# Optimization experiments

Measured on AMD Instinct MI355X. Metric: run time of the kernel, lower is better.

The kernel has to match this reference:

```python
import jax, jax.numpy as jnp
import numpy as np

B, N, V, H, R, A, IN, K = 64, 512, 64, 512, 4, 18, 128, 32
EPS = 1e-8


def setup_inputs() -> dict:
    key = jax.random.key(0)
    ks = jax.random.split(key, 20)
    g = lambda i, shape, s=1.0: jax.random.normal(ks[i], shape, jnp.float32) * s
    u = lambda i, shape: jax.random.uniform(ks[i], shape, dtype=jnp.float32)
    cin = IN + R * V
    return dict(
        x=g(0, (B, IN)),
        h=g(1, (B, H), 0.1),
        c=g(2, (B, H), 0.1),
        memory=g(3, (B, N, V), 0.1),
        read_weights=u(4, (B, R, N)),
        write_weights=u(5, (B, N)),
        usage=u(6, (B, N)),
        link_matrix=u(7, (B, N, N)) * 0.01,
        precedence_weights=u(8, (B, N)),
        W_ih=g(9, (4 * H, cin), 0.05), W_hh=g(10, (4 * H, H), 0.05),
        b_ih=jnp.zeros(4 * H, jnp.float32), b_hh=jnp.zeros(4 * H, jnp.float32),
        W_read=g(11, (R, V + 4, H), 0.05), b_read=jnp.zeros((R, V + 4), jnp.float32),
        W_write=g(12, (3 * V + 3, H), 0.05), b_write=jnp.zeros(3 * V + 3, jnp.float32),
        W_pol=g(13, (A, H), 0.05), b_pol=jnp.zeros(A, jnp.float32),
        W_val=g(14, (1, H), 0.05), b_val=jnp.zeros(1, jnp.float32),
    )


def reference(x, h, c, memory, read_weights, write_weights, usage, link_matrix,
              precedence_weights, W_ih, W_hh, b_ih, b_hh, W_read, b_read,
              W_write, b_write, W_pol, b_pol, W_val, b_val):
    # ---- read heads (vectorized over R) ----
    ro = jnp.einsum('roh,bh->bro', W_read, h) + b_read            # [B,R,V+4]
    rkey = ro[..., :V]
    rbeta = jax.nn.softplus(ro[..., V])                           # [B,R]
    rpi = jax.nn.softmax(ro[..., V + 1:V + 4], axis=-1)           # backward/content/forward gates
    mem_norm = jnp.maximum(jnp.linalg.norm(memory, axis=-1), EPS)  # [B,N]
    key_norm = jnp.maximum(jnp.linalg.norm(rkey, axis=-1), EPS)    # [B,R]
    sim = jnp.einsum('bnv,brv->brn', memory, rkey) / (mem_norm[:, None, :] * key_norm[..., None])
    scores = rbeta[..., None] * sim                                # [B,R,N]
    kth = jax.lax.top_k(scores, K)[0][..., -1:]                    # sparse top-k mask
    cw = jax.nn.softmax(jnp.where(scores >= kth, scores, -jnp.inf), axis=-1)
    fw = jnp.einsum('bnm,brm->brn', link_matrix, read_weights)     # forward weighting L w
    bw = jnp.einsum('bmn,brm->brn', link_matrix, read_weights)     # backward weighting L^T w
    w_r = rpi[..., 0:1] * bw + rpi[..., 1:2] * cw + rpi[..., 2:3] * fw  # [B,R,N]
    rvec = jnp.einsum('brn,bnv->brv', w_r, memory).reshape(B, R * V)
    # ---- LSTM controller (torch LSTMCell gate order i,f,g,o) ----
    gates = jnp.concatenate([x, rvec], -1) @ W_ih.T + h @ W_hh.T + b_ih + b_hh
    i_g, f_g, g_g, o_g = jnp.split(gates, 4, axis=-1)
    c_new = jax.nn.sigmoid(f_g) * c + jax.nn.sigmoid(i_g) * jnp.tanh(g_g)
    h_new = jax.nn.sigmoid(o_g) * jnp.tanh(c_new)
    # ---- write head ----
    wo = h_new @ W_write.T + b_write                               # [B,3V+3]
    wkey = wo[:, :V]
    erase = jax.nn.sigmoid(wo[:, V:2 * V])
    add = jnp.tanh(wo[:, 2 * V:3 * V])
    wbeta = jax.nn.softplus(wo[:, 3 * V])
    g_a = jax.nn.sigmoid(wo[:, 3 * V + 1])
    g_w = jax.nn.sigmoid(wo[:, 3 * V + 2])
    wkey_norm = jnp.maximum(jnp.linalg.norm(wkey, axis=-1), EPS)
    wsim = jnp.einsum('bnv,bv->bn', memory, wkey) / (mem_norm * wkey_norm[:, None])
    cw_w = jax.nn.softmax(wbeta[:, None] * wsim, axis=-1)
    # allocation weighting from sorted usage (DNC Eq. 1)
    idx = jnp.argsort(usage, axis=-1)
    u_sorted = jnp.take_along_axis(usage, idx, -1)
    prod_prev = jnp.concatenate([jnp.ones((B, 1), usage.dtype), jnp.cumprod(u_sorted, -1)[:, :-1]], -1)
    a_sorted = (1.0 - u_sorted) * prod_prev
    alloc = jnp.take_along_axis(a_sorted, jnp.argsort(idx, -1), -1)
    write_w = g_w[:, None] * (g_a[:, None] * alloc + (1.0 - g_a)[:, None] * cw_w)  # [B,N]
    # ---- memory erase/add ----
    mem_new = memory * (1.0 - write_w[:, :, None] * erase[:, None, :]) + write_w[:, :, None] * add[:, None, :]
    # ---- usage (psi detached as in torch.no_grad) ----
    psi = jax.lax.stop_gradient(jnp.prod(1.0 - w_r, axis=1))
    usage_new = (usage + write_weights - usage * write_weights) * psi
    # ---- link matrix + precedence ----
    ws = jnp.sum(write_w, -1, keepdims=True)
    prec_new = (1.0 - ws) * precedence_weights + write_w
    decay = (1.0 - write_w[:, :, None]) * (1.0 - write_w[:, None, :])
    link_new = decay * link_matrix + write_w[:, :, None] * precedence_weights[:, None, :]
    link_new = link_new * (1.0 - jnp.eye(N, dtype=link_new.dtype))
    # ---- actor/critic heads ----
    logits = h_new @ W_pol.T + b_pol
    value = h_new @ W_val.T + b_val
    return (logits, value, h_new, c_new, mem_new, w_r, write_w, usage_new, link_new, prec_new)
```

## Files before the change

kernel.cpp:

```cpp
#include <hip/hip_runtime.h>
#include <math.h>

constexpr int Bb = 64, Nn = 512, Vv = 64, Hh = 512, Rr = 4, Aa = 18, INp = 128, KTOP = 32;
constexpr int CIN = 384;
constexpr int WOUT = 195;
#define EPSf 1e-8f

__device__ __forceinline__ float sigmoidf(float x){ return 1.f/(1.f+expf(-x)); }
__device__ __forceinline__ float softplusf(float x){ return (x>20.f)? x : log1pf(expf(x)); }
__device__ __forceinline__ float wave_reduce(float v){
  #pragma unroll
  for(int o=32;o>0;o>>=1) v += __shfl_down(v, o, 64);
  return v;
}

__global__ void k_read_proj(const float* __restrict__ Wr, const float* __restrict__ br,
                            const float* __restrict__ h, float* __restrict__ ro) {
  int bid = blockIdx.x;
  int b = bid / 68;
  int p = (bid % 68) * 4 + (threadIdx.x >> 6);
  int lane = threadIdx.x & 63;
  const float* wrow = Wr + p * Hh;
  const float* hb = h + b * Hh;
  float acc = 0.f;
  #pragma unroll
  for (int t = 0; t < 8; ++t) { int k = lane + 64*t; acc += wrow[k] * hb[k]; }
  acc = wave_reduce(acc);
  if (lane == 0) ro[b*272 + p] = acc + br[p];
}

__global__ void k_scores(const float* __restrict__ mem, const float* __restrict__ ro,
                         float* __restrict__ scores) {
  int row = blockIdx.x*4 + (threadIdx.x>>6);
  int lane = threadIdx.x & 63;
  int b = row >> 9, n = row & 511;
  float m = mem[row*Vv + lane];
  float mn = wave_reduce(m*m);
  #pragma unroll
  for (int r = 0; r < Rr; ++r) {
    const float* rob = ro + b*272 + r*68;
    float kv = rob[lane];
    float s  = wave_reduce(m*kv);
    float k2 = wave_reduce(kv*kv);
    if (lane == 0) {
      float rbeta = softplusf(rob[64]);
      float mnc = fmaxf(sqrtf(mn), EPSf);
      float knc = fmaxf(sqrtf(k2), EPSf);
      scores[(b*Rr + r)*Nn + n] = rbeta * s / (mnc * knc);
    }
  }
}

__global__ void k_topk_cw(const float* __restrict__ scores, float* __restrict__ cw) {
  __shared__ float sv[512];
  __shared__ float so[512];
  __shared__ float red[256];
  int br = blockIdx.x;
  int tid = threadIdx.x;
  const float* srow = scores + br*Nn;
  for (int i = tid; i < 512; i += 256) { float v = srow[i]; sv[i]=v; so[i]=v; }
  __syncthreads();
  for (int k = 2; k <= 512; k <<= 1) {
    for (int j = k>>1; j > 0; j >>= 1) {
      for (int i = tid; i < 512; i += 256) {
        int ixj = i ^ j;
        if (ixj > i) {
          float a = sv[i], c = sv[ixj];
          bool descSeg = ((i & k) == 0);
          bool sw = descSeg ? (a < c) : (a > c);
          if (sw) { sv[i]=c; sv[ixj]=a; }
        }
      }
      __syncthreads();
    }
  }
  float kth = sv[KTOP-1];
  float mx = sv[0];
  float lsum = 0.f;
  for (int i = tid; i < 512; i += 256) {
    float v = so[i];
    lsum += (v >= kth) ? expf(v - mx) : 0.f;
  }
  red[tid] = lsum; __syncthreads();
  for (int s2 = 128; s2 > 0; s2 >>= 1) {
    if (tid < s2) red[tid] += red[tid+s2];
    __syncthreads();
  }
  float inv = 1.f / red[0];
  for (int i = tid; i < 512; i += 256) {
    float v = so[i];
    cw[br*Nn + i] = (v >= kth) ? expf(v - mx)*inv : 0.f;
  }
}

__global__ void k_fwbw(const float* __restrict__ link, const float* __restrict__ rw,
                       float* __restrict__ fw, float* __restrict__ bwpart) {
  __shared__ float bl[4][4][512];
  int b  = blockIdx.x >> 3;
  int ch = blockIdx.x & 7;
  int wv = threadIdx.x >> 6, lane = threadIdx.x & 63;
  const float* rwb = rw + b*Rr*Nn;
  float rwv[4][8];
  #pragma unroll
  for (int r = 0; r < 4; ++r)
    #pragma unroll
    for (int t = 0; t < 8; ++t) rwv[r][t] = rwb[r*512 + lane + 64*t];
  float bwacc[8][4] = {};
  const float* lb = link + (size_t)b*Nn*Nn;
  int n0 = ch*64 + wv*16;
  for (int i = 0; i < 16; ++i) {
    int n = n0 + i;
    float lk[8];
    #pragma unroll
    for (int t = 0; t < 8; ++t) lk[t] = lb[n*512 + lane + 64*t];
    float s0 = rwb[n], s1 = rwb[512+n], s2 = rwb[1024+n], s3 = rwb[1536+n];
    float f0=0,f1=0,f2=0,f3=0;
    #pragma unroll
    for (int t = 0; t < 8; ++t) {
      float lv = lk[t];
      f0 += lv*rwv[0][t]; f1 += lv*rwv[1][t]; f2 += lv*rwv[2][t]; f3 += lv*rwv[3][t];
      bwacc[t][0] += lv*s0; bwacc[t][1] += lv*s1; bwacc[t][2] += lv*s2; bwacc[t][3] += lv*s3;
    }
    f0 = wave_reduce(f0); f1 = wave_reduce(f1);
    f2 = wave_reduce(f2); f3 = wave_reduce(f3);
    if (lane == 0) {
      fw[(b*Rr+0)*Nn+n] = f0; fw[(b*Rr+1)*Nn+n] = f1;
      fw[(b*Rr+2)*Nn+n] = f2; fw[(b*Rr+3)*Nn+n] = f3;
    }
  }
  #pragma unroll
  for (int t = 0; t < 8; ++t)
    #pragma unroll
    for (int r = 0; r < 4; ++r) bl[wv][r][lane + 64*t] = bwacc[t][r];
  __syncthreads();
  int tid = threadIdx.x;
  #pragma unroll
  for (int q = 0; q < 8; ++q) {
    int idx = q*256 + tid;
    int r = idx >> 9, j = idx & 511;
    float v = bl[0][r][j] + bl[1][r][j] + bl[2][r][j] + bl[3][r][j];
    bwpart[((size_t)(ch*Bb + b)*Rr + r)*Nn + j] = v;
  }
}

__global__ void k_wr_usage(const float* __restrict__ bwpart, const float* __restrict__ cw,
                           const float* __restrict__ fw, const float* __restrict__ ro,
                           const float* __restrict__ usage, const float* __restrict__ wwt,
                           float* __restrict__ out_wr, float* __restrict__ out_usage,
                           float* __restrict__ ws_rvec) {
  int idx = blockIdx.x*256 + threadIdx.x;
  if (idx < Bb*Rr*Vv) ws_rvec[idx] = 0.f;
  int b = idx >> 9, n = idx & 511;
  float psi = 1.f;
  #pragma unroll
  for (int r = 0; r < Rr; ++r) {
    int br = b*Rr + r;
    const float* rob = ro + b*272 + r*68;
    float e0 = rob[65], e1 = rob[66], e2 = rob[67];
    float m = fmaxf(e0, fmaxf(e1, e2));
    float x0 = expf(e0-m), x1 = expf(e1-m), x2 = expf(e2-m);
    float inv = 1.f/(x0+x1+x2);
    float bwv = 0.f;
    #pragma unroll
    for (int chh = 0; chh < 8; ++chh)
      bwv += bwpart[((size_t)(chh*Bb + b)*Rr + r)*Nn + n];
    float w = (x0*bwv + x1*cw[br*Nn+n] + x2*fw[br*Nn+n]) * inv;
    out_wr[br*Nn+n] = w;
    psi *= (1.f - w);
  }
  float u = usage[idx], wt = wwt[idx];
  out_usage[idx] = (u + wt - u*wt) * psi;
}

__global__ void k_rvec(const float* __restrict__ wr, const float* __restrict__ mem,
                       float* __restrict__ rvec) {
  int b = blockIdx.x >> 3;
  int ch = blockIdx.x & 7;
  int r = threadIdx.x >> 6, v = threadIdx.x & 63;
  const float* wrow = wr + (b*Rr + r)*Nn;
  const float* mb = mem + (size_t)b*Nn*Vv;
  float acc = 0.f;
  #pragma unroll 4
  for (int t = 0; t < 64; ++t) {
    int n = ch*64 + t;
    acc += wrow[n] * mb[n*Vv + v];
  }
  atomicAdd(&rvec[(b*Rr+r)*Vv + v], acc);
}

__global__ void k_gates(const float* __restrict__ x, const float* __restrict__ rvec,
                        const float* __restrict__ h, const float* __restrict__ Wih,
                        const float* __restrict__ Whh, const float* __restrict__ bih,
                        const float* __restrict__ bhh, float* __restrict__ gates) {
  int gid = blockIdx.x*4 + (threadIdx.x>>6);
  int lane = threadIdx.x & 63;
  int jt = gid >> 4;
  int bt = gid & 15;
  float acc[4][4] = {};
  #pragma unroll
  for (int t = 0; t < 6; ++t) {
    int k = lane + 64*t;
    float u[4], w[4];
    #pragma unroll
    for (int i = 0; i < 4; ++i) {
      int b = bt*4 + i;
      u[i] = (k < INp) ? x[b*INp + k] : rvec[b*(Rr*Vv) + k - INp];
      w[i] = Wih[(jt*4+i)*CIN + k];
    }
    #pragma unroll
    for (int jj = 0; jj < 4; ++jj)
      #pragma unroll
      for (int bb = 0; bb < 4; ++bb) acc[jj][bb] += w[jj]*u[bb];
  }
  #pragma unroll
  for (int t = 0; t < 8; ++t) {
    int k = lane + 64*t;
    float u[4], w[4];
    #pragma unroll
    for (int i = 0; i < 4; ++i) {
      u[i] = h[(bt*4+i)*Hh + k];
      w[i] = Whh[(jt*4+i)*Hh + k];
    }
    #pragma unroll
    for (int jj = 0; jj < 4; ++jj)
      #pragma unroll
      for (int bb = 0; bb < 4; ++bb) acc[jj][bb] += w[jj]*u[bb];
  }
  #pragma unroll
  for (int jj = 0; jj < 4; ++jj)
    #pragma unroll
    for (int bb = 0; bb < 4; ++bb) {
      float v = wave_reduce(acc[jj][bb]);
      if (lane == 0) {
        int j = jt*4 + jj, b = bt*4 + bb;
        gates[b*(4*Hh) + j] = v + bih[j] + bhh[j];
      }
    }
}

__global__ void k_lstm(const float* __restrict__ gates, const float* __restrict__ c,
                       float* __restrict__ out_h, float* __restrict__ out_c) {
  int idx = blockIdx.x*256 + threadIdx.x;
  int b = idx >> 9, hh = idx & 511;
  const float* g = gates + b*2048;
  float ig = sigmoidf(g[hh]), fg = sigmoidf(g[512+hh]);
  float gg = tanhf(g[1024+hh]), og = sigmoidf(g[1536+hh]);
  float cn = fg * c[idx] + ig * gg;
  float hn = og * tanhf(cn);
  out_c[idx] = cn; out_h[idx] = hn;
}

__global__ void k_wopol(const float* __restrict__ hn, const float* __restrict__ Ww,
                        const float* __restrict__ bw_, const float* __restrict__ Wp,
                        const float* __restrict__ bp, const float* __restrict__ Wv,
                        const float* __restrict__ bv, float* __restrict__ wo,
                        float* __restrict__ out_logits, float* __restrict__ out_value) {
  int gid = blockIdx.x*4 + (threadIdx.x>>6);
  int lane = threadIdx.x & 63;
  int b = gid / 214, o = gid % 214;
  const float* wrow;
  if (o < WOUT) wrow = Ww + o*Hh;
  else if (o < WOUT + Aa) wrow = Wp + (o-WOUT)*Hh;
  else wrow = Wv;
  const float* hb = hn + b*Hh;
  float acc = 0.f;
  #pragma unroll
  for (int t = 0; t < 8; ++t) { int k = lane+64*t; acc += hb[k]*wrow[k]; }
  acc = wave_reduce(acc);
  if (lane == 0) {
    if (o < WOUT) wo[b*WOUT+o] = acc + bw_[o];
    else if (o < WOUT + Aa) out_logits[b*Aa + (o-WOUT)] = acc + bp[o-WOUT];
    else out_value[b] = acc + bv[0];
  }
}

__global__ void k_wsim(const float* __restrict__ mem, const float* __restrict__ wo,
                       float* __restrict__ wsim) {
  int row = blockIdx.x*4 + (threadIdx.x>>6);
  int lane = threadIdx.x & 63;
  int b = row >> 9;
  const float* wob = wo + b*WOUT;
  float kv = wob[lane];
  float m = mem[row*Vv + lane];
  float s  = wave_reduce(m*kv);
  float mn = wave_reduce(m*m);
  float k2 = wave_reduce(kv*kv);
  if (lane == 0) {
    float wbeta = softplusf(wob[192]);
    wsim[row] = wbeta * s / (fmaxf(sqrtf(mn),EPSf) * fmaxf(sqrtf(k2),EPSf));
  }
}

__global__ void k_alloc(const float* __restrict__ usage, const float* __restrict__ wo,
                        const float* __restrict__ wsim, const float* __restrict__ prec,
                        float* __restrict__ out_ww, float* __restrict__ out_prec) {
  __shared__ float uv[512];
  __shared__ int   ui[512];
  __shared__ float cp[512];
  __shared__ float al[512];
  __shared__ float red[256];
  int b = blockIdx.x, tid = threadIdx.x;
  float s0 = wsim[b*Nn + tid], s1 = wsim[b*Nn + tid + 256];
  red[tid] = fmaxf(s0, s1); __syncthreads();
  for (int s2=128; s2>0; s2>>=1){ if (tid<s2) red[tid]=fmaxf(red[tid],red[tid+s2]); __syncthreads(); }
  float mx = red[0]; __syncthreads();
  float e0 = expf(s0-mx), e1 = expf(s1-mx);
  red[tid] = e0+e1; __syncthreads();
  for (int s2=128; s2>0; s2>>=1){ if (tid<s2) red[tid]+=red[tid+s2]; __syncthreads(); }
  float cinv = 1.f/red[0];
  float c0 = e0*cinv, c1 = e1*cinv;
  __syncthreads();
  for (int i = tid; i < 512; i += 256) { uv[i] = usage[b*Nn+i]; ui[i] = i; }
  __syncthreads();
  for (int k = 2; k <= 512; k <<= 1) {
    for (int j = k>>1; j > 0; j >>= 1) {
      for (int i = tid; i < 512; i += 256) {
        int ixj = i ^ j;
        if (ixj > i) {
          float av = uv[i], bv = uv[ixj];
          int ai = ui[i], bi = ui[ixj];
          bool gt = (av > bv) || (av == bv && ai > bi);
          bool asc = ((i & k) == 0);
          bool sw = asc ? gt : !gt;
          if (sw) { uv[i]=bv; uv[ixj]=av; ui[i]=bi; ui[ixj]=ai; }
        }
      }
      __syncthreads();
    }
  }
  for (int i = tid; i < 512; i += 256) cp[i] = uv[i];
  __syncthreads();
  for (int d = 1; d < 512; d <<= 1) {
    float t0 = cp[tid]     * ((tid >= d)     ? cp[tid-d]     : 1.f);
    float t1 = cp[tid+256] * ((tid+256 >= d) ? cp[tid+256-d] : 1.f);
    __syncthreads();
    cp[tid] = t0; cp[tid+256] = t1;
    __syncthreads();
  }
  for (int i = tid; i < 512; i += 256) {
    float pp = (i == 0) ? 1.f : cp[i-1];
    al[ui[i]] = (1.f - uv[i]) * pp;
  }
  __syncthreads();
  float ga = sigmoidf(wo[b*WOUT+193]);
  float gw = sigmoidf(wo[b*WOUT+194]);
  int n0 = tid, n1 = tid+256;
  float wv0 = gw * (ga*al[n0] + (1.f-ga)*c0);
  float wv1 = gw * (ga*al[n1] + (1.f-ga)*c1);
  out_ww[b*Nn+n0] = wv0; out_ww[b*Nn+n1] = wv1;
  red[tid] = wv0 + wv1; __syncthreads();
  for (int s2=128; s2>0; s2>>=1){ if (tid<s2) red[tid]+=red[tid+s2]; __syncthreads(); }
  float wsum = red[0];
  out_prec[b*Nn+n0] = (1.f - wsum)*prec[b*Nn+n0] + wv0;
  out_prec[b*Nn+n1] = (1.f - wsum)*prec[b*Nn+n1] + wv1;
}

__global__ void k_memlink(const float* __restrict__ link, const float* __restrict__ ww,
                          const float* __restrict__ prec, const float* __restrict__ mem,
                          const float* __restrict__ wo, float* __restrict__ out_link,
                          float* __restrict__ out_mem) {
  int bid = blockIdx.x;
  if (bid < 16384) {
    int idx4 = bid*256 + threadIdx.x;
    int base = idx4*4;
    int b = base >> 18;
    int rem = base & 262143;
    int i = rem >> 9;
    int j0 = rem & 511;
    float wi = ww[b*Nn + i];
    float fi = 1.f - wi;
    float4 lv = *(const float4*)(link + base);
    float4 wj = *(const float4*)(ww + b*Nn + j0);
    float4 pj = *(const float4*)(prec + b*Nn + j0);
    float4 o;
    o.x = fi*(1.f-wj.x)*lv.x + wi*pj.x;
    o.y = fi*(1.f-wj.y)*lv.y + wi*pj.y;
    o.z = fi*(1.f-wj.z)*lv.z + wi*pj.z;
    o.w = fi*(1.f-wj.w)*lv.w + wi*pj.w;
    if (i >= j0 && i < j0+4) {
      if (i == j0) o.x = 0.f;
      else if (i == j0+1) o.y = 0.f;
      else if (i == j0+2) o.z = 0.f;
      else o.w = 0.f;
    }
    *(float4*)(out_link + base) = o;
  } else {
    int idx4 = (bid - 16384)*256 + threadIdx.x;
    int base = idx4*4;
    int b = base >> 15;
    int rem = base & 32767;
    int n = rem >> 6;
    int v0 = rem & 63;
    float w = ww[b*Nn + n];
    const float* wob = wo + b*WOUT;
    float4 m = *(const float4*)(mem + base);
    float4 o;
    float e, a;
    e = sigmoidf(wob[64+v0+0]); a = tanhf(wob[128+v0+0]); o.x = m.x*(1.f-w*e)+w*a;
    e = sigmoidf(wob[64+v0+1]); a = tanhf(wob[128+v0+1]); o.y = m.y*(1.f-w*e)+w*a;
    e = sigmoidf(wob[64+v0+2]); a = tanhf(wob[128+v0+2]); o.z = m.z*(1.f-w*e)+w*a;
    e = sigmoidf(wob[64+v0+3]); a = tanhf(wob[128+v0+3]); o.w = m.w*(1.f-w*e)+w*a;
    *(float4*)(out_mem + base) = o;
  }
}

extern "C" void kernel_launch(void* const* d_in, const int* in_sizes, int n_in,
                              void* d_out, int out_size, void* d_ws, size_t ws_size,
                              hipStream_t stream) {
  const float* x    = (const float*)d_in[0];
  const float* h    = (const float*)d_in[1];
  const float* c    = (const float*)d_in[2];
  const float* mem  = (const float*)d_in[3];
  const float* rw   = (const float*)d_in[4];
  const float* wwt  = (const float*)d_in[5];
  const float* usage= (const float*)d_in[6];
  const float* link = (const float*)d_in[7];
  const float* prec = (const float*)d_in[8];
  const float* Wih  = (const float*)d_in[9];
  const float* Whh  = (const float*)d_in[10];
  const float* bih  = (const float*)d_in[11];
  const float* bhh  = (const float*)d_in[12];
  const float* Wr   = (const float*)d_in[13];
  const float* br   = (const float*)d_in[14];
  const float* Ww   = (const float*)d_in[15];
  const float* bw_  = (const float*)d_in[16];
  const float* Wp   = (const float*)d_in[17];
  const float* bp   = (const float*)d_in[18];
  const float* Wv   = (const float*)d_in[19];
  const float* bv   = (const float*)d_in[20];

  float* out = (float*)d_out;
  float* o_logits = out + 0;
  float* o_value  = out + 1152;
  float* o_h      = out + 1216;
  float* o_c      = out + 33984;
  float* o_mem    = out + 66752;
  float* o_wr     = out + 2163904;
  float* o_ww     = out + 2294976;
  float* o_usage  = out + 2327744;
  float* o_link   = out + 2360512;
  float* o_prec   = out + 19137728;

  float* ws = (float*)d_ws;
  float* ws_ro     = ws;
  float* ws_sc     = ws + 17408;
  float* ws_cw     = ws + 148480;
  float* ws_fw     = ws + 279552;
  float* ws_bwpart = ws + 410624;
  float* ws_rvec   = ws + 1459200;
  float* ws_gates  = ws + 1475584;
  float* ws_wo     = ws + 1606656;
  float* ws_wsim   = ws + 1619136;

  k_read_proj <<<dim3(Bb*68),        dim3(256), 0, stream>>>(Wr, br, h, ws_ro);
  k_scores    <<<dim3(Bb*Nn/4),      dim3(256), 0, stream>>>(mem, ws_ro, ws_sc);
  k_topk_cw   <<<dim3(Bb*Rr),        dim3(256), 0, stream>>>(ws_sc, ws_cw);
  k_fwbw      <<<dim3(Bb*8),         dim3(256), 0, stream>>>(link, rw, ws_fw, ws_bwpart);
  k_wr_usage  <<<dim3(Bb*Nn/256),    dim3(256), 0, stream>>>(ws_bwpart, ws_cw, ws_fw, ws_ro, usage, wwt, o_wr, o_usage, ws_rvec);
  k_rvec      <<<dim3(Bb*8),         dim3(256), 0, stream>>>(o_wr, mem, ws_rvec);
  k_gates     <<<dim3(2048),         dim3(256), 0, stream>>>(x, ws_rvec, h, Wih, Whh, bih, bhh, ws_gates);
  k_lstm      <<<dim3(Bb*Hh/256),    dim3(256), 0, stream>>>(ws_gates, c, o_h, o_c);
  k_wopol     <<<dim3(Bb*214/4),     dim3(256), 0, stream>>>(o_h, Ww, bw_, Wp, bp, Wv, bv, ws_wo, o_logits, o_value);
  k_wsim      <<<dim3(Bb*Nn/4),      dim3(256), 0, stream>>>(mem, ws_wo, ws_wsim);
  k_alloc     <<<dim3(Bb),           dim3(256), 0, stream>>>(usage, ws_wo, ws_wsim, prec, o_ww, o_prec);
  k_memlink   <<<dim3(16384+2048),   dim3(256), 0, stream>>>(link, o_ww, prec, mem, ws_wo, o_link, o_mem);
}
```

Measured before the change: 345.2 us.

## Fuse all DNC stages into one cooperative persistent kernel with grid syncs

```diff
diff --git a/kernel.cpp b/kernel.cpp
--- a/kernel.cpp
+++ b/kernel.cpp
@@ -1,9 +1,15 @@
 #include <hip/hip_runtime.h>
+#include <hip/hip_cooperative_groups.h>
 #include <math.h>
+
+namespace cg = cooperative_groups;
 
 constexpr int Bb = 64, Nn = 512, Vv = 64, Hh = 512, Rr = 4, Aa = 18, INp = 128, KTOP = 32;
 constexpr int CIN = 384;
 constexpr int WOUT = 195;
+constexpr int GRID = 256;
+constexpr int NWAVE = GRID*4;
+constexpr int NTHRD = GRID*256;
 #define EPSf 1e-8f
 
 __device__ __forceinline__ float sigmoidf(float x){ return 1.f/(1.f+expf(-x)); }
@@ -14,393 +20,422 @@
   return v;
 }
 
-__global__ void k_read_proj(const float* __restrict__ Wr, const float* __restrict__ br,
-                            const float* __restrict__ h, float* __restrict__ ro) {
-  int bid = blockIdx.x;
-  int b = bid / 68;
-  int p = (bid % 68) * 4 + (threadIdx.x >> 6);
-  int lane = threadIdx.x & 63;
-  const float* wrow = Wr + p * Hh;
-  const float* hb = h + b * Hh;
-  float acc = 0.f;
-  #pragma unroll
-  for (int t = 0; t < 8; ++t) { int k = lane + 64*t; acc += wrow[k] * hb[k]; }
-  acc = wave_reduce(acc);
-  if (lane == 0) ro[b*272 + p] = acc + br[p];
-}
-
-__global__ void k_scores(const float* __restrict__ mem, const float* __restrict__ ro,
-                         float* __restrict__ scores) {
-  int row = blockIdx.x*4 + (threadIdx.x>>6);
-  int lane = threadIdx.x & 63;
-  int b = row >> 9, n = row & 511;
-  float m = mem[row*Vv + lane];
-  float mn = wave_reduce(m*m);
-  #pragma unroll
-  for (int r = 0; r < Rr; ++r) {
-    const float* rob = ro + b*272 + r*68;
-    float kv = rob[lane];
+constexpr int WS_RO     = 0;
+constexpr int WS_SC     = 17408;
+constexpr int WS_CW     = 148480;
+constexpr int WS_FW     = 279552;
+constexpr int WS_BWPART = 410624;
+constexpr int WS_RVEC   = 1459200;
+constexpr int WS_GATES  = 1475584;
+constexpr int WS_WO     = 1606656;
+constexpr int WS_WSIM   = 1619136;
+
+__global__ __launch_bounds__(256, 2) void dnc_mega(
+    const float* __restrict__ x, const float* __restrict__ h, const float* __restrict__ c,
+    const float* __restrict__ mem, const float* __restrict__ rw, const float* __restrict__ wwt,
+    const float* __restrict__ usage, const float* __restrict__ link, const float* __restrict__ prec,
+    const float* __restrict__ Wih, const float* __restrict__ Whh,
+    const float* __restrict__ bih, const float* __restrict__ bhh,
+    const float* __restrict__ Wr, const float* __restrict__ br,
+    const float* __restrict__ Ww, const float* __restrict__ bw_,
+    const float* __restrict__ Wp, const float* __restrict__ bp,
+    const float* __restrict__ Wv, const float* __restrict__ bv,
+    float* __restrict__ out, float* __restrict__ ws) {
+  cg::grid_group grid = cg::this_grid();
+  __shared__ __align__(16) char smem[32768];
+
+  const int tid = threadIdx.x;
+  const int wv = tid >> 6, lane = tid & 63;
+  const int blk = blockIdx.x;
+  const int gwave = blk*4 + wv;
+  const int gthread = blk*256 + tid;
+
+  float* o_logits = out + 0;
+  float* o_value  = out + 1152;
+  float* o_h      = out + 1216;
+  float* o_c      = out + 33984;
+  float* o_mem    = out + 66752;
+  float* o_wr     = out + 2163904;
+  float* o_ww     = out + 2294976;
+  float* o_usage  = out + 2327744;
+  float* o_link   = out + 2360512;
+  float* o_prec   = out + 19137728;
+
+  float* ws_ro     = ws + WS_RO;
+  float* ws_sc     = ws + WS_SC;
+  float* ws_cw     = ws + WS_CW;
+  float* ws_fw     = ws + WS_FW;
+  float* ws_bwpart = ws + WS_BWPART;
+  float* ws_rvec   = ws + WS_RVEC;
+  float* ws_gates  = ws + WS_GATES;
+  float* ws_wo     = ws + WS_WO;
+  float* ws_wsim   = ws + WS_WSIM;
+
+  for (int u = gwave; u < Bb*272; u += NWAVE) {
+    int b = u / 272, p = u % 272;
+    const float* wrow = Wr + p*Hh;
+    const float* hb = h + b*Hh;
+    float acc = 0.f;
+    #pragma unroll
+    for (int t = 0; t < 8; ++t) { int k = lane + 64*t; acc += wrow[k]*hb[k]; }
+    acc = wave_reduce(acc);
+    if (lane == 0) ws_ro[b*272 + p] = acc + br[p];
+  }
+  for (int unit = blk; unit < 512; unit += GRID) {
+    float (*bl)[4][512] = (float(*)[4][512])smem;
+    int b  = unit >> 3;
+    int ch = unit & 7;
+    const float* rwb = rw + b*Rr*Nn;
+    float rwv[4][8];
+    #pragma unroll
+    for (int r = 0; r < 4; ++r)
+      #pragma unroll
+      for (int t = 0; t < 8; ++t) rwv[r][t] = rwb[r*512 + lane + 64*t];
+    float bwacc[8][4] = {};
+    const float* lb = link + (size_t)b*Nn*Nn;
+    int n0 = ch*64 + wv*16;
+    for (int i = 0; i < 16; ++i) {
+      int n = n0 + i;
+      float lk[8];
+      #pragma unroll
+      for (int t = 0; t < 8; ++t) lk[t] = lb[n*512 + lane + 64*t];
+      float s0 = rwb[n], s1 = rwb[512+n], s2 = rwb[1024+n], s3 = rwb[1536+n];
+      float f0=0,f1=0,f2=0,f3=0;
+      #pragma unroll
+      for (int t = 0; t < 8; ++t) {
+        float lv = lk[t];
+        f0 += lv*rwv[0][t]; f1 += lv*rwv[1][t]; f2 += lv*rwv[2][t]; f3 += lv*rwv[3][t];
+        bwacc[t][0] += lv*s0; bwacc[t][1] += lv*s1; bwacc[t][2] += lv*s2; bwacc[t][3] += lv*s3;
+      }
+      f0 = wave_reduce(f0); f1 = wave_reduce(f1);
+      f2 = wave_reduce(f2); f3 = wave_reduce(f3);
+      if (lane == 0) {
+        ws_fw[(b*Rr+0)*Nn+n] = f0; ws_fw[(b*Rr+1)*Nn+n] = f1;
+        ws_fw[(b*Rr+2)*Nn+n] = f2; ws_fw[(b*Rr+3)*Nn+n] = f3;
+      }
+    }
+    #pragma unroll
+    for (int t = 0; t < 8; ++t)
+      #pragma unroll
+      for (int r = 0; r < 4; ++r) bl[wv][r][lane + 64*t] = bwacc[t][r];
+    __syncthreads();
+    #pragma unroll
+    for (int q = 0; q < 8; ++q) {
+      int idx = q*256 + tid;
+      int r = idx >> 9, j = idx & 511;
+      float v = bl[0][r][j] + bl[1][r][j] + bl[2][r][j] + bl[3][r][j];
+      ws_bwpart[((size_t)(ch*Bb + b)*Rr + r)*Nn + j] = v;
+    }
+    __syncthreads();
+  }
+  grid.sync();
+
+  for (int u = gwave; u < Bb*Nn; u += NWAVE) {
+    int b = u >> 9, n = u & 511;
+    float m = mem[u*Vv + lane];
+    float mn = wave_reduce(m*m);
+    #pragma unroll
+    for (int r = 0; r < Rr; ++r) {
+      float kv = ws_ro[b*272 + r*68 + lane];
+      float s = wave_reduce(m*kv);
+      if (lane == 0)
+        ws_sc[(b*Rr + r)*Nn + n] = s / fmaxf(sqrtf(mn), EPSf);
+    }
+  }
+  grid.sync();
+
+  {
+    float* sv = (float*)smem;
+    float* so = sv + 512;
+    float* red = so + 512;
+    float* sscale = red + 256;
+    int b = blk >> 2, r = blk & 3;
+    if (wv == 0) {
+      float kv = ws_ro[b*272 + r*68 + lane];
+      float k2 = wave_reduce(kv*kv);
+      if (lane == 0) {
+        float rbeta = softplusf(ws_ro[b*272 + r*68 + 64]);
+        *sscale = rbeta / fmaxf(sqrtf(k2), EPSf);
+      }
+    }
+    __syncthreads();
+    float scale = *sscale;
+    const float* srow = ws_sc + (b*Rr + r)*Nn;
+    for (int i = tid; i < 512; i += 256) { float v = scale*srow[i]; sv[i]=v; so[i]=v; }
+    __syncthreads();
+    for (int k = 2; k <= 512; k <<= 1) {
+      for (int j = k>>1; j > 0; j >>= 1) {
+        for (int i = tid; i < 512; i += 256) {
+          int ixj = i ^ j;
+          if (ixj > i) {
+            float a = sv[i], cc = sv[ixj];
+            bool descSeg = ((i & k) == 0);
+            bool sw = descSeg ? (a < cc) : (a > cc);
+            if (sw) { sv[i]=cc; sv[ixj]=a; }
+          }
+        }
+        __syncthreads();
+      }
+    }
+    float kth = sv[KTOP-1];
+    float mx = sv[0];
+    float lsum = 0.f;
+    for (int i = tid; i < 512; i += 256) {
+      float v = so[i];
+      lsum += (v >= kth) ? expf(v - mx) : 0.f;
+    }
+    red[tid] = lsum; __syncthreads();
+    for (int s2 = 128; s2 > 0; s2 >>= 1) {
+      if (tid < s2) red[tid] += red[tid+s2];
+      __syncthreads();
+    }
+    float inv = 1.f / red[0];
+    for (int i = tid; i < 512; i += 256) {
+      float v = so[i];
+      ws_cw[(b*Rr + r)*Nn + i] = (v >= kth) ? expf(v - mx)*inv : 0.f;
+    }
+    __syncthreads();
+  }
+  grid.sync();
+
+  if (gthread < Bb*Rr*Vv) ws_rvec[gthread] = 0.f;
+  if (gthread < Bb*Nn) {
+    int idx = gthread;
+    int b = idx >> 9, n = idx & 511;
+    float psi = 1.f;
+    #pragma unroll
+    for (int r = 0; r < Rr; ++r) {
+      int brr = b*Rr + r;
+      const float* rob = ws_ro + b*272 + r*68;
+      float e0 = rob[65], e1 = rob[66], e2 = rob[67];
+      float m = fmaxf(e0, fmaxf(e1, e2));
+      float x0 = expf(e0-m), x1 = expf(e1-m), x2 = expf(e2-m);
+      float inv = 1.f/(x0+x1+x2);
+      float bwv = 0.f;
+      #pragma unroll
+      for (int chh = 0; chh < 8; ++chh)
+        bwv += ws_bwpart[((size_t)(chh*Bb + b)*Rr + r)*Nn + n];
+      float w = (x0*bwv + x1*ws_cw[brr*Nn+n] + x2*ws_fw[brr*Nn+n]) * inv;
+      o_wr[brr*Nn+n] = w;
+      psi *= (1.f - w);
+    }
+    float u = usage[idx], wt = wwt[idx];
+    o_usage[idx] = (u + wt - u*wt) * psi;
+  }
+  grid.sync();
+
+  for (int unit = blk; unit < 512; unit += GRID) {
+    int b = unit >> 3;
+    int ch = unit & 7;
+    int r = wv, v = lane;
+    const float* wrow = o_wr + (b*Rr + r)*Nn;
+    const float* mb = mem + (size_t)b*Nn*Vv;
+    float acc = 0.f;
+    #pragma unroll 4
+    for (int t = 0; t < 64; ++t) {
+      int n = ch*64 + t;
+      acc += wrow[n] * mb[n*Vv + v];
+    }
+    atomicAdd(&ws_rvec[(b*Rr+r)*Vv + v], acc);
+  }
+  grid.sync();
+
+  for (int u = gwave; u < 8192; u += NWAVE) {
+    int jt = u >> 4;
+    int bt = u & 15;
+    float acc[4][4] = {};
+    #pragma unroll
+    for (int t = 0; t < 6; ++t) {
+      int k = lane + 64*t;
+      float uu[4], w[4];
+      #pragma unroll
+      for (int i = 0; i < 4; ++i) {
+        int b = bt*4 + i;
+        uu[i] = (k < INp) ? x[b*INp + k] : ws_rvec[b*(Rr*Vv) + k - INp];
+        w[i] = Wih[(jt*4+i)*CIN + k];
+      }
+      #pragma unroll
+      for (int jj = 0; jj < 4; ++jj)
+        #pragma unroll
+        for (int bb2 = 0; bb2 < 4; ++bb2) acc[jj][bb2] += w[jj]*uu[bb2];
+    }
+    #pragma unroll
+    for (int t = 0; t < 8; ++t) {
+      int k = lane + 64*t;
+      float uu[4], w[4];
+      #pragma unroll
+      for (int i = 0; i < 4; ++i) {
+        uu[i] = h[(bt*4+i)*Hh + k];
+        w[i] = Whh[(jt*4+i)*Hh + k];
+      }
+      #pragma unroll
+      for (int jj = 0; jj < 4; ++jj)
+        #pragma unroll
+        for (int bb2 = 0; bb2 < 4; ++bb2) acc[jj][bb2] += w[jj]*uu[bb2];
+    }
+    #pragma unroll
+    for (int jj = 0; jj < 4; ++jj)
+      #pragma unroll
+      for (int bb2 = 0; bb2 < 4; ++bb2) {
+        float v = wave_reduce(acc[jj][bb2]);
+        if (lane == 0) {
+          int j = jt*4 + jj, b = bt*4 + bb2;
+          ws_gates[b*(4*Hh) + j] = v + bih[j] + bhh[j];
+        }
+      }
+  }
+  grid.sync();
+
+  if (gthread < Bb*Hh) {
+    int idx = gthread;
+    int b = idx >> 9, hh = idx & 511;
+    const float* g = ws_gates + b*2048;
+    float ig = sigmoidf(g[hh]), fg = sigmoidf(g[512+hh]);
+    float gg = tanhf(g[1024+hh]), og = sigmoidf(g[1536+hh]);
+    float cn = fg * c[idx] + ig * gg;
+    float hn = og * tanhf(cn);
+    o_c[idx] = cn; o_h[idx] = hn;
+  }
+  grid.sync();
+
+  for (int u = gwave; u < Bb*214; u += NWAVE) {
+    int b = u / 214, o = u % 214;
+    const float* wrow;
+    if (o < WOUT) wrow = Ww + o*Hh;
+    else if (o < WOUT + Aa) wrow = Wp + (o-WOUT)*Hh;
+    else wrow = Wv;
+    const float* hb = o_h + b*Hh;
+    float acc = 0.f;
+    #pragma unroll
+    for (int t = 0; t < 8; ++t) { int k = lane+64*t; acc += hb[k]*wrow[k]; }
+    acc = wave_reduce(acc);
+    if (lane == 0) {
+      if (o < WOUT) ws_wo[b*WOUT+o] = acc + bw_[o];
+      else if (o < WOUT + Aa) o_logits[b*Aa + (o-WOUT)] = acc + bp[o-WOUT];
+      else o_value[b] = acc + bv[0];
+    }
+  }
+  grid.sync();
+
+  for (int u = gwave; u < Bb*Nn; u += NWAVE) {
+    int b = u >> 9;
+    const float* wob = ws_wo + b*WOUT;
+    float kv = wob[lane];
+    float m = mem[u*Vv + lane];
     float s  = wave_reduce(m*kv);
+    float mn = wave_reduce(m*m);
     float k2 = wave_reduce(kv*kv);
     if (lane == 0) {
-      float rbeta = softplusf(rob[64]);
-      float mnc = fmaxf(sqrtf(mn), EPSf);
-      float knc = fmaxf(sqrtf(k2), EPSf);
-      scores[(b*Rr + r)*Nn + n] = rbeta * s / (mnc * knc);
-    }
-  }
-}
-
-__global__ void k_topk_cw(const float* __restrict__ scores, float* __restrict__ cw) {
-  __shared__ float sv[512];
-  __shared__ float so[512];
-  __shared__ float red[256];
-  int br = blockIdx.x;
-  int tid = threadIdx.x;
-  const float* srow = scores + br*Nn;
-  for (int i = tid; i < 512; i += 256) { float v = srow[i]; sv[i]=v; so[i]=v; }
-  __syncthreads();
-  for (int k = 2; k <= 512; k <<= 1) {
-    for (int j = k>>1; j > 0; j >>= 1) {
-      for (int i = tid; i < 512; i += 256) {
-        int ixj = i ^ j;
-        if (ixj > i) {
-          float a = sv[i], c = sv[ixj];
-          bool descSeg = ((i & k) == 0);
-          bool sw = descSeg ? (a < c) : (a > c);
-          if (sw) { sv[i]=c; sv[ixj]=a; }
+      float wbeta = softplusf(wob[192]);
+      ws_wsim[u] = wbeta * s / (fmaxf(sqrtf(mn),EPSf) * fmaxf(sqrtf(k2),EPSf));
+    }
+  }
+  grid.sync();
+
+  if (blk < 64) {
+    float* uv = (float*)smem;
+    int*   ui = (int*)(uv + 512);
+    float* cp = (float*)(ui + 512);
+    float* al = cp + 512;
+    float* red = al + 512;
+    int b = blk;
+    float s0 = ws_wsim[b*Nn + tid], s1 = ws_wsim[b*Nn + tid + 256];
+    red[tid] = fmaxf(s0, s1); __syncthreads();
+    for (int s2=128; s2>0; s2>>=1){ if (tid<s2) red[tid]=fmaxf(red[tid],red[tid+s2]); __syncthreads(); }
+    float mx = red[0]; __syncthreads();
+    float e0 = expf(s0-mx), e1 = expf(s1-mx);
+    red[tid] = e0+e1; __syncthreads();
+    for (int s2=128; s2>0; s2>>=1){ if (tid<s2) red[tid]+=red[tid+s2]; __syncthreads(); }
+    float cinv = 1.f/red[0];
+    float c0 = e0*cinv, c1 = e1*cinv;
+    __syncthreads();
+    for (int i = tid; i < 512; i += 256) { uv[i] = usage[b*Nn+i]; ui[i] = i; }
+    __syncthreads();
+    for (int k = 2; k <= 512; k <<= 1) {
+      for (int j = k>>1; j > 0; j >>= 1) {
+        for (int i = tid; i < 512; i += 256) {
+          int ixj = i ^ j;
+          if (ixj > i) {
+            float av = uv[i], bv2 = uv[ixj];
+            int ai = ui[i], bi = ui[ixj];
+            bool gt = (av > bv2) || (av == bv2 && ai > bi);
+            bool asc = ((i & k) == 0);
+            bool sw = asc ? gt : !gt;
+            if (sw) { uv[i]=bv2; uv[ixj]=av; ui[i]=bi; ui[ixj]=ai; }
+          }
         }
-      }
+        __syncthreads();
+      }
+    }
+    for (int i = tid; i < 512; i += 256) cp[i] = uv[i];
+    __syncthreads();
+    for (int d = 1; d < 512; d <<= 1) {
+      float t0 = cp[tid]     * ((tid >= d)     ? cp[tid-d]     : 1.f);
+      float t1 = cp[tid+256] * ((tid+256 >= d) ? cp[tid+256-d] : 1.f);
       __syncthreads();
-    }
-  }
-  float kth = sv[KTOP-1];
-  float mx = sv[0];
-  float lsum = 0.f;
-  for (int i = tid; i < 512; i += 256) {
-    float v = so[i];
-    lsum += (v >= kth) ? expf(v - mx) : 0.f;
-  }
-  red[tid] = lsum; __syncthreads();
-  for (int s2 = 128; s2 > 0; s2 >>= 1) {
-    if (tid < s2) red[tid] += red[tid+s2];
-    __syncthreads();
-  }
-  float inv = 1.f / red[0];
-  for (int i = tid; i < 512; i += 256) {
-    float v = so[i];
-    cw[br*Nn + i] = (v >= kth) ? expf(v - mx)*inv : 0.f;
-  }
-}
-
-__global__ void k_fwbw(const float* __restrict__ link, const float* __restrict__ rw,
-                       float* __restrict__ fw, float* __restrict__ bwpart) {
-  __shared__ float bl[4][4][512];
-  int b  = blockIdx.x >> 3;
-  int ch = blockIdx.x & 7;
-  int wv = threadIdx.x >> 6, lane = threadIdx.x & 63;
-  const float* rwb = rw + b*Rr*Nn;
-  float rwv[4][8];
-  #pragma unroll
-  for (int r = 0; r < 4; ++r)
-    #pragma unroll
-    for (int t = 0; t < 8; ++t) rwv[r][t] = rwb[r*512 + lane + 64*t];
-  float bwacc[8][4] = {};
-  const float* lb = link + (size_t)b*Nn*Nn;
-  int n0 = ch*64 + wv*16;
-  for (int i = 0; i < 16; ++i) {
-    int n = n0 + i;
-    float lk[8];
-    #pragma unroll
-    for (int t = 0; t < 8; ++t) lk[t] = lb[n*512 + lane + 64*t];
-    float s0 = rwb[n], s1 = rwb[512+n], s2 = rwb[1024+n], s3 = rwb[1536+n];
-    float f0=0,f1=0,f2=0,f3=0;
-    #pragma unroll
-    for (int t = 0; t < 8; ++t) {
-      float lv = lk[t];
-      f0 += lv*rwv[0][t]; f1 += lv*rwv[1][t]; f2 += lv*rwv[2][t]; f3 += lv*rwv[3][t];
-      bwacc[t][0] += lv*s0; bwacc[t][1] += lv*s1; bwacc[t][2] += lv*s2; bwacc[t][3] += lv*s3;
-    }
-    f0 = wave_reduce(f0); f1 = wave_reduce(f1);
-    f2 = wave_reduce(f2); f3 = wave_reduce(f3);
-    if (lane == 0) {
-      fw[(b*Rr+0)*Nn+n] = f0; fw[(b*Rr+1)*Nn+n] = f1;
-      fw[(b*Rr+2)*Nn+n] = f2; fw[(b*Rr+3)*Nn+n] = f3;
-    }
-  }
-  #pragma unroll
-  for (int t = 0; t < 8; ++t)
-    #pragma unroll
-    for (int r = 0; r < 4; ++r) bl[wv][r][lane + 64*t] = bwacc[t][r];
-  __syncthreads();
-  int tid = threadIdx.x;
-  #pragma unroll
-  for (int q = 0; q < 8; ++q) {
-    int idx = q*256 + tid;
-    int r = idx >> 9, j = idx & 511;
-    float v = bl[0][r][j] + bl[1][r][j] + bl[2][r][j] + bl[3][r][j];
-    bwpart[((size_t)(ch*Bb + b)*Rr + r)*Nn + j] = v;
-  }
-}
-
-__global__ void k_wr_usage(const float* __restrict__ bwpart, const float* __restrict__ cw,
-                           const float* __restrict__ fw, const float* __restrict__ ro,
-                           const float* __restrict__ usage, const float* __restrict__ wwt,
-                           float* __restrict__ out_wr, float* __restrict__ out_usage,
-                           float* __restrict__ ws_rvec) {
-  int idx = blockIdx.x*256 + threadIdx.x;
-  if (idx < Bb*Rr*Vv) ws_rvec[idx] = 0.f;
-  int b = idx >> 9, n = idx & 511;
-  float psi = 1.f;
-  #pragma unroll
-  for (int r = 0; r < Rr; ++r) {
-    int br = b*Rr + r;
-    const float* rob = ro + b*272 + r*68;
-    float e0 = rob[65], e1 = rob[66], e2 = rob[67];
-    float m = fmaxf(e0, fmaxf(e1, e2));
-    float x0 = expf(e0-m), x1 = expf(e1-m), x2 = expf(e2-m);
-    float inv = 1.f/(x0+x1+x2);
-    float bwv = 0.f;
-    #pragma unroll
-    for (int chh = 0; chh < 8; ++chh)
-      bwv += bwpart[((size_t)(chh*Bb + b)*Rr + r)*Nn + n];
-    float w = (x0*bwv + x1*cw[br*Nn+n] + x2*fw[br*Nn+n]) * inv;
-    out_wr[br*Nn+n] = w;
-    psi *= (1.f - w);
-  }
-  float u = usage[idx], wt = wwt[idx];
-  out_usage[idx] = (u + wt - u*wt) * psi;
-}
-
-__global__ void k_rvec(const float* __restrict__ wr, const float* __restrict__ mem,
-                       float* __restrict__ rvec) {
-  int b = blockIdx.x >> 3;
-  int ch = blockIdx.x & 7;
-  int r = threadIdx.x >> 6, v = threadIdx.x & 63;
-  const float* wrow = wr + (b*Rr + r)*Nn;
-  const float* mb = mem + (size_t)b*Nn*Vv;
-  float acc = 0.f;
-  #pragma unroll 4
-  for (int t = 0; t < 64; ++t) {
-    int n = ch*64 + t;
-    acc += wrow[n] * mb[n*Vv + v];
-  }
-  atomicAdd(&rvec[(b*Rr+r)*Vv + v], acc);
-}
-
-__global__ void k_gates(const float* __restrict__ x, const float* __restrict__ rvec,
-                        const float* __restrict__ h, const float* __restrict__ Wih,
-                        const float* __restrict__ Whh, const float* __restrict__ bih,
-                        const float* __restrict__ bhh, float* __restrict__ gates) {
-  int gid = blockIdx.x*4 + (threadIdx.x>>6);
-  int lane = threadIdx.x & 63;
-  int jt = gid >> 4;
-  int bt = gid & 15;
-  float acc[4][4] = {};
-  #pragma unroll
-  for (int t = 0; t < 6; ++t) {
-    int k = lane + 64*t;
-    float u[4], w[4];
-    #pragma unroll
-    for (int i = 0; i < 4; ++i) {
-      int b = bt*4 + i;
-      u[i] = (k < INp) ? x[b*INp + k] : rvec[b*(Rr*Vv) + k - INp];
-      w[i] = Wih[(jt*4+i)*CIN + k];
-    }
-    #pragma unroll
-    for (int jj = 0; jj < 4; ++jj)
-      #pragma unroll
-      for (int bb = 0; bb < 4; ++bb) acc[jj][bb] += w[jj]*u[bb];
-  }
-  #pragma unroll
-  for (int t = 0; t < 8; ++t) {
-    int k = lane + 64*t;
-    float u[4], w[4];
-    #pragma unroll
-    for (int i = 0; i < 4; ++i) {
-      u[i] = h[(bt*4+i)*Hh + k];
-      w[i] = Whh[(jt*4+i)*Hh + k];
-    }
-    #pragma unroll
-    for (int jj = 0; jj < 4; ++jj)
-      #pragma unroll
-      for (int bb = 0; bb < 4; ++bb) acc[jj][bb] += w[jj]*u[bb];
-  }
-  #pragma unroll
-  for (int jj = 0; jj < 4; ++jj)
-    #pragma unroll
-    for (int bb = 0; bb < 4; ++bb) {
-      float v = wave_reduce(acc[jj][bb]);
-      if (lane == 0) {
-        int j = jt*4 + jj, b = bt*4 + bb;
-        gates[b*(4*Hh) + j] = v + bih[j] + bhh[j];
-      }
-    }
-}
-
-__global__ void k_lstm(const float* __restrict__ gates, const float* __restrict__ c,
-                       float* __restrict__ out_h, float* __restrict__ out_c) {
-  int idx = blockIdx.x*256 + threadIdx.x;
-  int b = idx >> 9, hh = idx & 511;
-  const float* g = gates + b*2048;
-  float ig = sigmoidf(g[hh]), fg = sigmoidf(g[512+hh]);
-  float gg = tanhf(g[1024+hh]), og = sigmoidf(g[1536+hh]);
-  float cn = fg * c[idx] + ig * gg;
-  float hn = og * tanhf(cn);
-  out_c[idx] = cn; out_h[idx] = hn;
-}
-
-__global__ void k_wopol(const float* __restrict__ hn, const float* __restrict__ Ww,
-                        const float* __restrict__ bw_, const float* __restrict__ Wp,
-                        const float* __restrict__ bp, const float* __restrict__ Wv,
-                        const float* __restrict__ bv, float* __restrict__ wo,
-                        float* __restrict__ out_logits, float* __restrict__ out_value) {
-  int gid = blockIdx.x*4 + (threadIdx.x>>6);
-  int lane = threadIdx.x & 63;
-  int b = gid / 214, o = gid % 214;
-  const float* wrow;
-  if (o < WOUT) wrow = Ww + o*Hh;
-  else if (o < WOUT + Aa) wrow = Wp + (o-WOUT)*Hh;
-  else wrow = Wv;
-  const float* hb = hn + b*Hh;
-  float acc = 0.f;
-  #pragma unroll
-  for (int t = 0; t < 8; ++t) { int k = lane+64*t; acc += hb[k]*wrow[k]; }
-  acc = wave_reduce(acc);
-  if (lane == 0) {
-    if (o < WOUT) wo[b*WOUT+o] = acc + bw_[o];
-    else if (o < WOUT + Aa) out_logits[b*Aa + (o-WOUT)] = acc + bp[o-WOUT];
-    else out_value[b] = acc + bv[0];
-  }
-}
-
-__global__ void k_wsim(const float* __restrict__ mem, const float* __restrict__ wo,
-                       float* __restrict__ wsim) {
-  int row = blockIdx.x*4 + (threadIdx.x>>6);
-  int lane = threadIdx.x & 63;
-  int b = row >> 9;
-  const float* wob = wo + b*WOUT;
-  float kv = wob[lane];
-  float m = mem[row*Vv + lane];
-  float s  = wave_reduce(m*kv);
-  float mn = wave_reduce(m*m);
-  float k2 = wave_reduce(kv*kv);
-  if (lane == 0) {
-    float wbeta = softplusf(wob[192]);
-    wsim[row] = wbeta * s / (fmaxf(sqrtf(mn),EPSf) * fmaxf(sqrtf(k2),EPSf));
-  }
-}
-
-__global__ void k_alloc(const float* __restrict__ usage, const float* __restrict__ wo,
-                        const float* __restrict__ wsim, const float* __restrict__ prec,
-                        float* __restrict__ out_ww, float* __restrict__ out_prec) {
-  __shared__ float uv[512];
-  __shared__ int   ui[512];
-  __shared__ float cp[512];
-  __shared__ float al[512];
-  __shared__ float red[256];
-  int b = blockIdx.x, tid = threadIdx.x;
-  float s0 = wsim[b*Nn + tid], s1 = wsim[b*Nn + tid + 256];
-  red[tid] = fmaxf(s0, s1); __syncthreads();
-  for (int s2=128; s2>0; s2>>=1){ if (tid<s2) red[tid]=fmaxf(red[tid],red[tid+s2]); __syncthreads(); }
-  float mx = red[0]; __syncthreads();
-  float e0 = expf(s0-mx), e1 = expf(s1-mx);
-  red[tid] = e0+e1; __syncthreads();
-  for (int s2=128; s2>0; s2>>=1){ if (tid<s2) red[tid]+=red[tid+s2]; __syncthreads(); }
-  float cinv = 1.f/red[0];
-  float c0 = e0*cinv, c1 = e1*cinv;
-  __syncthreads();
-  for (int i = tid; i < 512; i += 256) { uv[i] = usage[b*Nn+i]; ui[i] = i; }
-  __syncthreads();
-  for (int k = 2; k <= 512; k <<= 1) {
-    for (int j = k>>1; j > 0; j >>= 1) {
-      for (int i = tid; i < 512; i += 256) {
-        int ixj = i ^ j;
-        if (ixj > i) {
-          float av = uv[i], bv = uv[ixj];
-          int ai = ui[i], bi = ui[ixj];
-          bool gt = (av > bv) || (av == bv && ai > bi);
-          bool asc = ((i & k) == 0);
-          bool sw = asc ? gt : !gt;
-          if (sw) { uv[i]=bv; uv[ixj]=av; ui[i]=bi; ui[ixj]=ai; }
-        }
-      }
+      cp[tid] = t0; cp[tid+256] = t1;
       __syncthreads();
     }
-  }
-  for (int i = tid; i < 512; i += 256) cp[i] = uv[i];
-  __syncthreads();
-  for (int d = 1; d < 512; d <<= 1) {
-    float t0 = cp[tid]     * ((tid >= d)     ? cp[tid-d]     : 1.f);
-    float t1 = cp[tid+256] * ((tid+256 >= d) ? cp[tid+256-d] : 1.f);
-    __syncthreads();
-    cp[tid] = t0; cp[tid+256] = t1;
-    __syncthreads();
-  }
-  for (int i = tid; i < 512; i += 256) {
-    float pp = (i == 0) ? 1.f : cp[i-1];
-    al[ui[i]] = (1.f - uv[i]) * pp;
-  }
-  __syncthreads();
-  float ga = sigmoidf(wo[b*WOUT+193]);
-  float gw = sigmoidf(wo[b*WOUT+194]);
-  int n0 = tid, n1 = tid+256;
-  float wv0 = gw * (ga*al[n0] + (1.f-ga)*c0);
-  float wv1 = gw * (ga*al[n1] + (1.f-ga)*c1);
-  out_ww[b*Nn+n0] = wv0; out_ww[b*Nn+n1] = wv1;
-  red[tid] = wv0 + wv1; __syncthreads();
-  for (int s2=128; s2>0; s2>>=1){ if (tid<s2) red[tid]+=red[tid+s2]; __syncthreads(); }
-  float wsum = red[0];
-  out_prec[b*Nn+n0] = (1.f - wsum)*prec[b*Nn+n0] + wv0;
-  out_prec[b*Nn+n1] = (1.f - wsum)*prec[b*Nn+n1] + wv1;
-}
-
-__global__ void k_memlink(const float* __restrict__ link, const float* __restrict__ ww,
-                          const float* __restrict__ prec, const float* __restrict__ mem,
-                          const float* __restrict__ wo, float* __restrict__ out_link,
-                          float* __restrict__ out_mem) {
-  int bid = blockIdx.x;
-  if (bid < 16384) {
-    int idx4 = bid*256 + threadIdx.x;
-    int base = idx4*4;
-    int b = base >> 18;
-    int rem = base & 262143;
-    int i = rem >> 9;
-    int j0 = rem & 511;
-    float wi = ww[b*Nn + i];
-    float fi = 1.f - wi;
-    float4 lv = *(const float4*)(link + base);
-    float4 wj = *(const float4*)(ww + b*Nn + j0);
-    float4 pj = *(const float4*)(prec + b*Nn + j0);
-    float4 o;
-    o.x = fi*(1.f-wj.x)*lv.x + wi*pj.x;
-    o.y = fi*(1.f-wj.y)*lv.y + wi*pj.y;
-    o.z = fi*(1.f-wj.z)*lv.z + wi*pj.z;
-    o.w = fi*(1.f-wj.w)*lv.w + wi*pj.w;
-    if (i >= j0 && i < j0+4) {
-      if (i == j0) o.x = 0.f;
-      else if (i == j0+1) o.y = 0.f;
-      else if (i == j0+2) o.z = 0.f;
-      else o.w = 0.f;
-    }
-    *(float4*)(out_link + base) = o;
-  } else {
-    int idx4 = (bid - 16384)*256 + threadIdx.x;
-    int base = idx4*4;
-    int b = base >> 15;
-    int rem = base & 32767;
-    int n = rem >> 6;
-    int v0 = rem & 63;
-    float w = ww[b*Nn + n];
-    const float* wob = wo + b*WOUT;
-    float4 m = *(const float4*)(mem + base);
-    float4 o;
-    float e, a;
-    e = sigmoidf(wob[64+v0+0]); a = tanhf(wob[128+v0+0]); o.x = m.x*(1.f-w*e)+w*a;
-    e = sigmoidf(wob[64+v0+1]); a = tanhf(wob[128+v0+1]); o.y = m.y*(1.f-w*e)+w*a;
-    e = sigmoidf(wob[64+v0+2]); a = tanhf(wob[128+v0+2]); o.z = m.z*(1.f-w*e)+w*a;
-    e = sigmoidf(wob[64+v0+3]); a = tanhf(wob[128+v0+3]); o.w = m.w*(1.f-w*e)+w*a;
-    *(float4*)(out_mem + base) = o;
+    for (int i = tid; i < 512; i += 256) {
+      float pp = (i == 0) ? 1.f : cp[i-1];
+      al[ui[i]] = (1.f - uv[i]) * pp;
+    }
+    __syncthreads();
+    float ga = sigmoidf(ws_wo[b*WOUT+193]);
+    float gw = sigmoidf(ws_wo[b*WOUT+194]);
+    int n0 = tid, n1 = tid+256;
+    float wv0 = gw * (ga*al[n0] + (1.f-ga)*c0);
+    float wv1 = gw * (ga*al[n1] + (1.f-ga)*c1);
+    o_ww[b*Nn+n0] = wv0; o_ww[b*Nn+n1] = wv1;
+    red[tid] = wv0 + wv1; __syncthreads();
+    for (int s2=128; s2>0; s2>>=1){ if (tid<s2) red[tid]+=red[tid+s2]; __syncthreads(); }
+    float wsum = red[0];
+    o_prec[b*Nn+n0] = (1.f - wsum)*prec[b*Nn+n0] + wv0;
+    o_prec[b*Nn+n1] = (1.f - wsum)*prec[b*Nn+n1] + wv1;
+  }
+  grid.sync();
+
+  for (int u = gthread; u < 4718592; u += NTHRD) {
+    if (u < 4194304) {
+      int base = u*4;
+      int b = base >> 18;
+      int rem = base & 262143;
+      int i = rem >> 9;
+      int j0 = rem & 511;
+      float wi = o_ww[b*Nn + i];
+      float fi = 1.f - wi;
+      float4 lv = *(const float4*)(link + base);
+      float4 wj = *(const float4*)(o_ww + b*Nn + j0);
+      float4 pj = *(const float4*)(prec + b*Nn + j0);
+      float4 o;
+      o.x = fi*(1.f-wj.x)*lv.x + wi*pj.x;
+      o.y = fi*(1.f-wj.y)*lv.y + wi*pj.y;
+      o.z = fi*(1.f-wj.z)*lv.z + wi*pj.z;
+      o.w = fi*(1.f-wj.w)*lv.w + wi*pj.w;
+      if (i >= j0 && i < j0+4) {
+        if (i == j0) o.x = 0.f;
+        else if (i == j0+1) o.y = 0.f;
+        else if (i == j0+2) o.z = 0.f;
+        else o.w = 0.f;
+      }
+      *(float4*)(o_link + base) = o;
+    } else {
+      int base = (u - 4194304)*4;
+      int b = base >> 15;
+      int rem = base & 32767;
+      int v0 = rem & 63;
+      int n = rem >> 6;
+      float w = o_ww[b*Nn + n];
+      const float* wob = ws_wo + b*WOUT;
+      float4 m = *(const float4*)(mem + base);
+      float4 o;
+      float e, a;
+      e = sigmoidf(wob[64+v0+0]); a = tanhf(wob[128+v0+0]); o.x = m.x*(1.f-w*e)+w*a;
+      e = sigmoidf(wob[64+v0+1]); a = tanhf(wob[128+v0+1]); o.y = m.y*(1.f-w*e)+w*a;
+      e = sigmoidf(wob[64+v0+2]); a = tanhf(wob[128+v0+2]); o.z = m.z*(1.f-w*e)+w*a;
+      e = sigmoidf(wob[64+v0+3]); a = tanhf(wob[128+v0+3]); o.w = m.w*(1.f-w*e)+w*a;
+      *(float4*)(o_mem + base) = o;
+    }
   }
 }
 
@@ -428,40 +463,14 @@
   const float* bp   = (const float*)d_in[18];
   const float* Wv   = (const float*)d_in[19];
   const float* bv   = (const float*)d_in[20];
-
   float* out = (float*)d_out;
-  float* o_logits = out + 0;
-  float* o_value  = out + 1152;
-  float* o_h      = out + 1216;
-  float* o_c      = out + 33984;
-  float* o_mem    = out + 66752;
-  float* o_wr     = out + 2163904;
-  float* o_ww     = out + 2294976;
-  float* o_usage  = out + 2327744;
-  float* o_link   = out + 2360512;
-  float* o_prec   = out + 19137728;
-
-  float* ws = (float*)d_ws;
-  float* ws_ro     = ws;
-  float* ws_sc     = ws + 17408;
-  float* ws_cw     = ws + 148480;
-  float* ws_fw     = ws + 279552;
-  float* ws_bwpart = ws + 410624;
-  float* ws_rvec   = ws + 1459200;
-  float* ws_gates  = ws + 1475584;
-  float* ws_wo     = ws + 1606656;
-  float* ws_wsim   = ws + 1619136;
-
-  k_read_proj <<<dim3(Bb*68),        dim3(256), 0, stream>>>(Wr, br, h, ws_ro);
-  k_scores    <<<dim3(Bb*Nn/4),      dim3(256), 0, stream>>>(mem, ws_ro, ws_sc);
-  k_topk_cw   <<<dim3(Bb*Rr),        dim3(256), 0, stream>>>(ws_sc, ws_cw);
-  k_fwbw      <<<dim3(Bb*8),         dim3(256), 0, stream>>>(link, rw, ws_fw, ws_bwpart);
-  k_wr_usage  <<<dim3(Bb*Nn/256),    dim3(256), 0, stream>>>(ws_bwpart, ws_cw, ws_fw, ws_ro, usage, wwt, o_wr, o_usage, ws_rvec);
-  k_rvec      <<<dim3(Bb*8),         dim3(256), 0, stream>>>(o_wr, mem, ws_rvec);
-  k_gates     <<<dim3(2048),         dim3(256), 0, stream>>>(x, ws_rvec, h, Wih, Whh, bih, bhh, ws_gates);
-  k_lstm      <<<dim3(Bb*Hh/256),    dim3(256), 0, stream>>>(ws_gates, c, o_h, o_c);
-  k_wopol     <<<dim3(Bb*214/4),     dim3(256), 0, stream>>>(o_h, Ww, bw_, Wp, bp, Wv, bv, ws_wo, o_logits, o_value);
-  k_wsim      <<<dim3(Bb*Nn/4),      dim3(256), 0, stream>>>(mem, ws_wo, ws_wsim);
-  k_alloc     <<<dim3(Bb),           dim3(256), 0, stream>>>(usage, ws_wo, ws_wsim, prec, o_ww, o_prec);
-  k_memlink   <<<dim3(16384+2048),   dim3(256), 0, stream>>>(link, o_ww, prec, mem, ws_wo, o_link, o_mem);
+  float* ws  = (float*)d_ws;
+
+  void* kargs[] = {
+    (void*)&x, (void*)&h, (void*)&c, (void*)&mem, (void*)&rw, (void*)&wwt,
+    (void*)&usage, (void*)&link, (void*)&prec, (void*)&Wih, (void*)&Whh,
+    (void*)&bih, (void*)&bhh, (void*)&Wr, (void*)&br, (void*)&Ww, (void*)&bw_,
+    (void*)&Wp, (void*)&bp, (void*)&Wv, (void*)&bv, (void*)&out, (void*)&ws
+  };
+  hipLaunchCooperativeKernel((void*)dnc_mega, dim3(GRID), dim3(256), kargs, 0, stream);
 }
```

Result: slower. 760.1 us (+120.2%).
